# Kernel optimization log

Measured on AMD Instinct MI355X. Metric: run time of the kernel, lower is better.

## Reference

```python
import jax, jax.numpy as jnp
import numpy as np

RADIUS = 0.4
K = 32
EPS = 1e-5


def ball_query(xyz, new_xyz, radius, k):
    """xyz: (B,N,3), new_xyz: (B,M,3) -> idx (B,M,k) int32.
    Replicates CUDA ball_query: first k points within radius (in index order),
    padded with the first found index."""
    N = xyz.shape[1]
    # squared distances (B,M,N)
    d2 = jnp.sum((new_xyz[:, :, None, :] - xyz[:, None, :, :]) ** 2, axis=-1)
    within = d2 < radius * radius
    order = jnp.arange(N, dtype=jnp.int32)
    key = jnp.where(within, order[None, None, :], N)
    idx_sorted = jnp.argsort(key, axis=-1)[..., :k].astype(jnp.int32)  # (B,M,k)
    cnt = within.sum(axis=-1)  # (B,M)
    first = idx_sorted[..., :1]
    slot = jnp.arange(k)[None, None, :]
    return jnp.where(slot < cnt[..., None], idx_sorted, first)


def gather_bmk(x_bnc, idx):
    """x_bnc: (B,N,C), idx: (B,M,K) -> (B,M,K,C)"""
    return jnp.take_along_axis(x_bnc[:, None, :, :], idx[..., None], axis=2)


def conv_bn_relu(x, w, b, gamma, beta):
    """x: (B,Cin,M,K); w: (Cout,Cin). 1x1 Conv2d + BatchNorm2d (train stats) + ReLU."""
    x = jnp.einsum('bcmk,oc->bomk', x, w) + b[None, :, None, None]
    mu = x.mean(axis=(0, 2, 3), keepdims=True)
    var = x.var(axis=(0, 2, 3), keepdims=True)
    x = gamma[None, :, None, None] * (x - mu) * jax.lax.rsqrt(var + EPS) + beta[None, :, None, None]
    return jax.nn.relu(x)


def setup_inputs() -> dict:
    key = jax.random.key(0)
    ks = jax.random.split(key, 16)
    B, N, C, M = 4, 16384, 128, 1024
    mlp = [131, 128, 128, 256]
    inp = {
        'points_xyz': jax.random.normal(ks[0], (B, N, 3), dtype=jnp.float32),
        'features': jax.random.normal(ks[1], (B, C, N), dtype=jnp.float32),
        'indices': jax.random.randint(ks[2], (B, M), 0, N, dtype=jnp.int32),
    }
    for i in range(3):
        cin, cout = mlp[i], mlp[i + 1]
        inp[f'w{i+1}'] = jax.random.normal(ks[3 + 4 * i], (cout, cin), dtype=jnp.float32) / np.sqrt(cin)
        inp[f'b{i+1}'] = jnp.zeros((cout,), dtype=jnp.float32)
        inp[f'g{i+1}'] = jnp.ones((cout,), dtype=jnp.float32)
        inp[f'beta{i+1}'] = jnp.zeros((cout,), dtype=jnp.float32)
    return inp


def reference(points_xyz, features, indices,
              w1, b1, g1, beta1, w2, b2, g2, beta2, w3, b3, g3, beta3):
    # sample centers: new_xyz (B,M,3)
    new_xyz = jnp.take_along_axis(points_xyz, indices[..., None], axis=1)
    # ball query + group
    idx = ball_query(points_xyz, new_xyz, RADIUS, K)            # (B,M,K)
    grouped_xyz = gather_bmk(points_xyz, idx) - new_xyz[:, :, None, :]  # (B,M,K,3)
    grouped_feat = gather_bmk(features.transpose(0, 2, 1), idx)         # (B,M,K,C)
    x = jnp.concatenate([grouped_xyz, grouped_feat], axis=-1)           # (B,M,K,3+C)
    x = x.transpose(0, 3, 1, 2)                                         # (B,3+C,M,K)
    # shared MLP (1x1 Conv2d + BN + ReLU)
    x = conv_bn_relu(x, w1, b1, g1, beta1)
    x = conv_bn_relu(x, w2, b2, g2, beta2)
    x = conv_bn_relu(x, w3, b3, g3, beta3)
    # max pool over K -> (B, Cout, M)
    new_features = x.max(axis=-1)
    return new_xyz, new_features
```

## Files before the change

kernel.cpp:

```cpp
#include <hip/hip_runtime.h>

#define B_ 4
#define N_ 16384
#define C_ 128
#define M_ 1024
#define K_ 32
#define NTOT (B_*M_*K_)
#define RAD2 0.16f
#define EPS_ 1e-5f

typedef unsigned short ushort_t;
typedef __bf16 bf16x8 __attribute__((ext_vector_type(8)));
typedef float f32x4 __attribute__((ext_vector_type(4)));

__device__ __forceinline__ float b2f(ushort_t u){
  unsigned int x = ((unsigned int)u) << 16;
  return __builtin_bit_cast(float, x);
}
__device__ __forceinline__ ushort_t f2b(float f){
  return __builtin_bit_cast(ushort_t, (__bf16)f);
}

__global__ __launch_bounds__(256) void prep_all_k(
    const float* __restrict__ feat, ushort_t* __restrict__ ftr_t,
    const float* __restrict__ xyz, const int* __restrict__ indices,
    float* __restrict__ new_xyz, int* __restrict__ idx,
    const float* __restrict__ w1, const float* __restrict__ w2, const float* __restrict__ w3,
    ushort_t* __restrict__ W1b, ushort_t* __restrict__ W2b, ushort_t* __restrict__ W3b,
    float* __restrict__ stats)
{
  __shared__ float T[32][133];
  int bid = blockIdx.x;
  int t = threadIdx.x;

  if (bid < 2048){
    int b = bid >> 9, ntile = bid & 511;
    int n0 = ntile * 32;
    int nl = t & 31;
    #pragma unroll
    for (int ci = 0; ci < 16; ci++){
      int c = ci*8 + (t >> 5);
      T[nl][c] = feat[((size_t)b*C_ + c)*N_ + n0 + nl];
    }
    __syncthreads();
    #pragma unroll
    for (int ii = 0; ii < 2; ii++){
      int v = ii*256 + t;
      int n2 = v >> 4, seg = v & 15;
      union { ushort_t u[8]; uint4 q; } pk;
      #pragma unroll
      for (int j = 0; j < 8; j++) pk.u[j] = f2b(T[n2][seg*8 + j]);
      *(uint4*)(ftr_t + ((size_t)b*N_ + n0 + n2)*C_ + seg*8) = pk.q;
    }
  } else if (bid < 3072){
    int wv = t >> 6, lane = t & 63;
    int g = (bid - 2048)*4 + wv;
    int b = g >> 10;
    const float* pb = xyz + (size_t)b*N_*3;
    const float4* pb4 = (const float4*)pb;
    int qi = indices[g];
    float qx = pb[qi*3+0], qy = pb[qi*3+1], qz = pb[qi*3+2];
    if (lane < 3) new_xyz[g*3 + lane] = pb[qi*3 + lane];

    int cnt = 0, firstIdx = 0;
    int* op = idx + g*K_;

    float4 buf0[6], buf1[6];
    #pragma unroll
    for (int i = 0; i < 6; i++) buf0[i] = pb4[lane*6 + i];

    auto process = [&](const float4* buf, int chunk){
      const float* f = (const float*)buf;
      unsigned int local_mask = 0;
      #pragma unroll
      for (int j = 0; j < 8; j++){
        float dx = f[j*3+0]-qx, dy = f[j*3+1]-qy, dz = f[j*3+2]-qz;
        if (dx*dx + dy*dy + dz*dz < RAD2) local_mask |= (1u << j);
      }
      if (__ballot(local_mask != 0) == 0ull) return;
      int base = chunk*512;
      int lcnt = __popc(local_mask);
      int incl = lcnt;
      #pragma unroll
      for (int d = 1; d < 64; d <<= 1){
        int tt = __shfl_up(incl, d);
        if (lane >= d) incl += tt;
      }
      int excl = incl - lcnt;
      int total = __shfl(incl, 63);
      if (cnt == 0){
        int lf = local_mask ? (lane*8 + __builtin_ctz(local_mask)) : 0x7fffffff;
        #pragma unroll
        for (int d = 1; d < 64; d <<= 1) lf = min(lf, __shfl_xor(lf, d));
        firstIdx = base + lf;
      }
      int sl = cnt + excl;
      unsigned int m = local_mask;
      while (m && sl < K_){
        int j = __builtin_ctz(m); m &= m - 1u;
        op[sl++] = base + lane*8 + j;
      }
      cnt += total;
    };

    for (int chunk = 0; chunk < 32; chunk += 2){
      if (chunk + 1 < 32){
        #pragma unroll
        for (int i = 0; i < 6; i++) buf1[i] = pb4[(chunk+1)*384 + lane*6 + i];
      }
      process(buf0, chunk);
      if (cnt >= K_) break;
      if (chunk + 2 < 32){
        #pragma unroll
        for (int i = 0; i < 6; i++) buf0[i] = pb4[(chunk+2)*384 + lane*6 + i];
      }
      process(buf1, chunk + 1);
      if (cnt >= K_) break;
    }
    if (cnt < K_){
      for (int s = cnt + lane; s < K_; s += 64) op[s] = firstIdx;
    }
  } else {
    const int T1 = 128*160, T2 = 128*128;
    int e = (bid - 3072)*256 + t;
    if (e < T1){
      int o = e / 160, c = e % 160;
      float v = 0.f;
      if (c < 128) v = w1[o*131 + 3 + c];
      else if (c < 131) v = w1[o*131 + (c - 128)];
      W1b[e] = f2b(v);
    } else if (e < T1+T2){
      int e2 = e - T1;
      W2b[e2] = f2b(w2[e2]);
    } else {
      int e3 = e - T1 - T2;
      W3b[e3] = f2b(w3[e3]);
    }
    if (bid == 3072){
      #pragma unroll
      for (int j = 0; j < 6; j++) stats[j*256 + t] = 0.f;
    }
  }
}

__global__ __launch_bounds__(256, 2) void conv1_k(
    const float* __restrict__ xyz, const ushort_t* __restrict__ ftr_t,
    const int* __restrict__ idx, const float* __restrict__ new_xyz,
    const ushort_t* __restrict__ W1b, const float* __restrict__ b1,
    ushort_t* __restrict__ Y1, float* __restrict__ sumO, float* __restrict__ sqO)
{
  __shared__ alignas(16) ushort_t Xs[2][32*168];
  __shared__ alignas(16) float Ys[2][32*68];
  int t = threadIdx.x;
  int wv = t >> 6, lane = t & 63, quad = lane >> 4, l15 = lane & 15;
  int row = t >> 3, chunk = t & 7;
  int col0 = (blockIdx.x & 1) * 64;
  int blk = blockIdx.x >> 1;

  if (t < 128){
    int rr = t >> 2, cc = t & 3;
    *(uint4*)(Xs[0] + rr*168 + 128 + cc*8) = make_uint4(0,0,0,0);
    *(uint4*)(Xs[1] + rr*168 + 128 + cc*8) = make_uint4(0,0,0,0);
  }
  bf16x8 wf[5];
  #pragma unroll
  for (int kt = 0; kt < 5; kt++)
    wf[kt] = *(const bf16x8*)(W1b + (col0 + wv*16 + l15)*160 + kt*32 + quad*8);
  float bs_r = b1[col0 + wv*16 + l15];
  float s = 0.f, s2 = 0.f;

  const int GPB = 8;
  int g0 = blk * GPB;
  int b = g0 >> 10;
  int ia[GPB], ibv[GPB];
  #pragma unroll
  for (int i = 0; i < GPB; i++){
    ia[i]  = idx[(g0+i)*K_ + row];
    ibv[i] = idx[(g0+i)*K_ + (t & 31)];
  }
  uint4 r0, r1;
  float p3x, p3y, p3z, q3x, q3y, q3z;
  {
    const ushort_t* src = ftr_t + ((size_t)b*N_ + ia[0])*C_ + chunk*16;
    r0 = *(const uint4*)src; r1 = *(const uint4*)(src + 8);
    if (t < 32){
      const float* pp = xyz + ((size_t)b*N_ + ibv[0])*3;
      const float* qq = new_xyz + (size_t)g0*3;
      p3x = pp[0]; p3y = pp[1]; p3z = pp[2];
      q3x = qq[0]; q3y = qq[1]; q3z = qq[2];
    }
  }
  for (int i = 0; i < GPB; i++){
    int p = i & 1;
    ushort_t* X = Xs[p];
    *(uint4*)(X + row*168 + chunk*16) = r0;
    *(uint4*)(X + row*168 + chunk*16 + 8) = r1;
    if (t < 32){
      unsigned int u0 = (unsigned int)f2b(p3x-q3x) | ((unsigned int)f2b(p3y-q3y) << 16);
      unsigned int u1 = (unsigned int)f2b(p3z-q3z);
      *(uint2*)(X + t*168 + 128) = make_uint2(u0, u1);
    }
    if (i + 1 < GPB){
      const ushort_t* src = ftr_t + ((size_t)b*N_ + ia[i+1])*C_ + chunk*16;
      r0 = *(const uint4*)src; r1 = *(const uint4*)(src + 8);
      if (t < 32){
        const float* pp = xyz + ((size_t)b*N_ + ibv[i+1])*3;
        const float* qq = new_xyz + (size_t)(g0+i+1)*3;
        p3x = pp[0]; p3y = pp[1]; p3z = pp[2];
        q3x = qq[0]; q3y = qq[1]; q3z = qq[2];
      }
    }
    __syncthreads();
    bf16x8 af[2][5];
    #pragma unroll
    for (int mt = 0; mt < 2; mt++)
      #pragma unroll
      for (int kt = 0; kt < 5; kt++)
        af[mt][kt] = *(const bf16x8*)(X + (mt*16 + l15)*168 + kt*32 + quad*8);
    f32x4 acc[2] = {(f32x4){0,0,0,0}, (f32x4){0,0,0,0}};
    #pragma unroll
    for (int kt = 0; kt < 5; kt++){
      acc[0] = __builtin_amdgcn_mfma_f32_16x16x32_bf16(af[0][kt], wf[kt], acc[0], 0,0,0);
      acc[1] = __builtin_amdgcn_mfma_f32_16x16x32_bf16(af[1][kt], wf[kt], acc[1], 0,0,0);
    }
    {
      int o = wv*16 + l15;
      float* Yw = Ys[p];
      #pragma unroll
      for (int mt = 0; mt < 2; mt++)
        #pragma unroll
        for (int r = 0; r < 4; r++){
          float v = acc[mt][r] + bs_r;
          s += v; s2 += v*v;
          Yw[(mt*16 + quad*4 + r)*68 + o] = v;
        }
    }
    if (i > 0){
      const float* yp = &Ys[p^1][row*68 + chunk*8];
      f32x4 y0 = *(const f32x4*)(yp);
      f32x4 y1 = *(const f32x4*)(yp + 4);
      union { ushort_t u[8]; uint4 q; } p0;
      #pragma unroll
      for (int j = 0; j < 4; j++){
        p0.u[j] = f2b(y0[j]); p0.u[4+j] = f2b(y1[j]);
      }
      *(uint4*)(Y1 + ((size_t)(g0+i-1)*K_ + row)*128 + col0 + chunk*8) = p0.q;
    }
  }
  __syncthreads();
  {
    const float* yp = &Ys[(GPB-1)&1][row*68 + chunk*8];
    f32x4 y0 = *(const f32x4*)(yp);
    f32x4 y1 = *(const f32x4*)(yp + 4);
    union { ushort_t u[8]; uint4 q; } p0;
    #pragma unroll
    for (int j = 0; j < 4; j++){
      p0.u[j] = f2b(y0[j]); p0.u[4+j] = f2b(y1[j]);
    }
    *(uint4*)(Y1 + ((size_t)(g0+GPB-1)*K_ + row)*128 + col0 + chunk*8) = p0.q;
  }
  s  += __shfl_xor(s, 16);  s  += __shfl_xor(s, 32);
  s2 += __shfl_xor(s2, 16); s2 += __shfl_xor(s2, 32);
  if (quad == 0){
    int o = col0 + wv*16 + l15;
    atomicAdd(&sumO[o], s);
    atomicAdd(&sqO[o], s2);
  }
}

template<int COUT, bool MAXMIN>
__global__ __launch_bounds__(256, 2) void convB_k(
    const ushort_t* __restrict__ Yin, const ushort_t* __restrict__ Wb,
    const float* __restrict__ bias, const float* __restrict__ g_bn,
    const float* __restrict__ beta_bn, const float* __restrict__ sumI,
    const float* __restrict__ sqI, ushort_t* __restrict__ Yout,
    unsigned int* __restrict__ Ymm, float* __restrict__ sumO, float* __restrict__ sqO)
{
  constexpr int HALF = COUT/2;
  constexpr int NT = HALF/64;
  __shared__ alignas(16) ushort_t Xs[2][32*136];
  __shared__ alignas(16) float Ys[MAXMIN ? 1 : 2][MAXMIN ? 4 : 32*68];
  int t = threadIdx.x;
  int wv = t >> 6, lane = t & 63, quad = lane >> 4, l15 = lane & 15;
  int row = t >> 3, chunk = t & 7;
  int col0 = (blockIdx.x & 1) * HALF;
  int blk = blockIdx.x >> 1;

  float a_r[16], d_r[16];
  #pragma unroll
  for (int j = 0; j < 16; j++){
    int c = chunk*16 + j;
    float mu  = sumI[c] * (1.f/NTOT);
    float var = sqI[c]  * (1.f/NTOT) - mu*mu;
    float a = g_bn[c] * rsqrtf(var + EPS_);
    a_r[j] = a; d_r[j] = beta_bn[c] - a*mu;
  }
  bf16x8 wf[NT][4];
  #pragma unroll
  for (int nt = 0; nt < NT; nt++)
    #pragma unroll
    for (int kt = 0; kt < 4; kt++)
      wf[nt][kt] = *(const bf16x8*)(Wb + (col0 + wv*(NT*16) + nt*16 + l15)*128 + kt*32 + quad*8);
  float bs_r[NT];
  #pragma unroll
  for (int nt = 0; nt < NT; nt++) bs_r[nt] = bias[col0 + wv*(NT*16) + nt*16 + l15];
  float s[NT], s2[NT];
  #pragma unroll
  for (int nt = 0; nt < NT; nt++){ s[nt] = 0.f; s2[nt] = 0.f; }

  const int GPB = 8;
  int g0 = blk * GPB;
  uint4 r0, r1;
  {
    const ushort_t* src = Yin + ((size_t)g0*K_ + row)*128 + chunk*16;
    r0 = *(const uint4*)src; r1 = *(const uint4*)(src + 8);
  }
  for (int i = 0; i < GPB; i++){
    int p = i & 1;
    int g = g0 + i;
    ushort_t* X = Xs[p];
    union { ushort_t u[8]; uint4 q; } i0, i1, o0, o1;
    i0.q = r0; i1.q = r1;
    #pragma unroll
    for (int j = 0; j < 8; j++){
      o0.u[j] = f2b(fmaxf(a_r[j]  *b2f(i0.u[j]) + d_r[j],   0.f));
      o1.u[j] = f2b(fmaxf(a_r[8+j]*b2f(i1.u[j]) + d_r[8+j], 0.f));
    }
    *(uint4*)(X + row*136 + chunk*16) = o0.q;
    *(uint4*)(X + row*136 + chunk*16 + 8) = o1.q;
    if (i + 1 < GPB){
      const ushort_t* src = Yin + ((size_t)(g+1)*K_ + row)*128 + chunk*16;
      r0 = *(const uint4*)src; r1 = *(const uint4*)(src + 8);
    }
    __syncthreads();
    bf16x8 af[2][4];
    #pragma unroll
    for (int mt = 0; mt < 2; mt++)
      #pragma unroll
      for (int kt = 0; kt < 4; kt++)
        af[mt][kt] = *(const bf16x8*)(X + (mt*16 + l15)*136 + kt*32 + quad*8);
    f32x4 acc[NT][2];
    #pragma unroll
    for (int nt = 0; nt < NT; nt++){ acc[nt][0] = (f32x4){0,0,0,0}; acc[nt][1] = (f32x4){0,0,0,0}; }
    #pragma unroll
    for (int nt = 0; nt < NT; nt++)
      #pragma unroll
      for (int kt = 0; kt < 4; kt++){
        acc[nt][0] = __builtin_amdgcn_mfma_f32_16x16x32_bf16(af[0][kt], wf[nt][kt], acc[nt][0], 0,0,0);
        acc[nt][1] = __builtin_amdgcn_mfma_f32_16x16x32_bf16(af[1][kt], wf[nt][kt], acc[nt][1], 0,0,0);
      }
    if constexpr (!MAXMIN){
      {
        int o = wv*16 + l15;
        float* Yw = Ys[p];
        #pragma unroll
        for (int mt = 0; mt < 2; mt++)
          #pragma unroll
          for (int r = 0; r < 4; r++){
            float v = acc[0][mt][r] + bs_r[0];
            s[0] += v; s2[0] += v*v;
            Yw[(mt*16 + quad*4 + r)*68 + o] = v;
          }
      }
      if (i > 0){
        const float* yp = &Ys[p^1][row*68 + chunk*8];
        f32x4 y0 = *(const f32x4*)(yp);
        f32x4 y1 = *(const f32x4*)(yp + 4);
        union { ushort_t u[8]; uint4 q; } p0;
        #pragma unroll
        for (int j = 0; j < 4; j++){
          p0.u[j] = f2b(y0[j]); p0.u[4+j] = f2b(y1[j]);
        }
        *(uint4*)(Yout + ((size_t)(g-1)*K_ + row)*128 + col0 + chunk*8) = p0.q;
      }
    } else {
      #pragma unroll
      for (int nt = 0; nt < NT; nt++){
        float v0 = acc[nt][0][0] + bs_r[nt];
        float mx = v0, mn = v0;
        s[nt] += v0; s2[nt] += v0*v0;
        #pragma unroll
        for (int mt = 0; mt < 2; mt++)
          #pragma unroll
          for (int r = 0; r < 4; r++){
            if (mt == 0 && r == 0) continue;
            float v = acc[nt][mt][r] + bs_r[nt];
            s[nt] += v; s2[nt] += v*v;
            mx = fmaxf(mx, v); mn = fminf(mn, v);
          }
        mx = fmaxf(mx, __shfl_xor(mx, 16)); mx = fmaxf(mx, __shfl_xor(mx, 32));
        mn = fminf(mn, __shfl_xor(mn, 16)); mn = fminf(mn, __shfl_xor(mn, 32));
        if (quad == 0){
          int o = col0 + wv*(NT*16) + nt*16 + l15;
          Ymm[(size_t)g*256 + o] = (unsigned int)f2b(mx) | ((unsigned int)f2b(mn) << 16);
        }
      }
    }
  }
  if constexpr (!MAXMIN){
    __syncthreads();
    const float* yp = &Ys[(GPB-1)&1][row*68 + chunk*8];
    f32x4 y0 = *(const f32x4*)(yp);
    f32x4 y1 = *(const f32x4*)(yp + 4);
    union { ushort_t u[8]; uint4 q; } p0;
    #pragma unroll
    for (int j = 0; j < 4; j++){
      p0.u[j] = f2b(y0[j]); p0.u[4+j] = f2b(y1[j]);
    }
    *(uint4*)(Yout + ((size_t)(g0+GPB-1)*K_ + row)*128 + col0 + chunk*8) = p0.q;
  }
  #pragma unroll
  for (int nt = 0; nt < NT; nt++){
    s[nt]  += __shfl_xor(s[nt], 16);  s[nt]  += __shfl_xor(s[nt], 32);
    s2[nt] += __shfl_xor(s2[nt], 16); s2[nt] += __shfl_xor(s2[nt], 32);
    if (quad == 0){
      int o = col0 + wv*(NT*16) + nt*16 + l15;
      atomicAdd(&sumO[o], s[nt]);
      atomicAdd(&sqO[o], s2[nt]);
    }
  }
}

__global__ __launch_bounds__(256) void finalize_k(
    const unsigned int* __restrict__ Ymm, const float* __restrict__ g3,
    const float* __restrict__ beta3, const float* __restrict__ sum3,
    const float* __restrict__ sq3, float* __restrict__ out)
{
  __shared__ float T[16][264];
  __shared__ float abn[256], dbn[256];
  int t = threadIdx.x;
  int b = blockIdx.x >> 6;
  int m0 = (blockIdx.x & 63) * 16;
  {
    float mu  = sum3[t] * (1.f/NTOT);
    float var = sq3[t]  * (1.f/NTOT) - mu*mu;
    float a = g3[t] * rsqrtf(var + EPS_);
    abn[t] = a; dbn[t] = beta3[t] - a*mu;
  }
  __syncthreads();
  #pragma unroll
  for (int i = 0; i < 4; i++){
    int v4 = i*256 + t;
    int m = v4 >> 6, oq = (v4 & 63) * 4;
    uint4 w = *(const uint4*)(Ymm + ((size_t)(b*M_ + m0 + m))*256 + oq);
    unsigned int wsv[4] = {w.x, w.y, w.z, w.w};
    float r[4];
    #pragma unroll
    for (int j = 0; j < 4; j++){
      int o = oq + j;
      float mx = b2f((ushort_t)(wsv[j] & 0xffffu));
      float mn = b2f((ushort_t)(wsv[j] >> 16));
      float a = abn[o];
      float val = (a >= 0.f) ? (a*mx + dbn[o]) : (a*mn + dbn[o]);
      r[j] = fmaxf(val, 0.f);
    }
    *(f32x4*)(&T[m][oq]) = *(f32x4*)r;
  }
  __syncthreads();
  #pragma unroll
  for (int p = 0; p < 4; p++){
    int o = p*64 + (t >> 2), c = t & 3;
    float4 v = make_float4(T[c*4+0][o], T[c*4+1][o], T[c*4+2][o], T[c*4+3][o]);
    *(float4*)(out + ((size_t)(b*256 + o))*M_ + m0 + c*4) = v;
  }
}

extern "C" void kernel_launch(void* const* d_in, const int* in_sizes, int n_in,
                              void* d_out, int out_size, void* d_ws, size_t ws_size,
                              hipStream_t stream)
{
  (void)in_sizes; (void)n_in; (void)out_size; (void)ws_size;
  const float* xyz  = (const float*)d_in[0];
  const float* feat = (const float*)d_in[1];
  const int*   inds = (const int*)d_in[2];
  const float* w1 = (const float*)d_in[3];
  const float* b1 = (const float*)d_in[4];
  const float* g1 = (const float*)d_in[5];
  const float* be1= (const float*)d_in[6];
  const float* w2 = (const float*)d_in[7];
  const float* b2 = (const float*)d_in[8];
  const float* g2 = (const float*)d_in[9];
  const float* be2= (const float*)d_in[10];
  const float* w3 = (const float*)d_in[11];
  const float* b3 = (const float*)d_in[12];
  const float* g3 = (const float*)d_in[13];
  const float* be3= (const float*)d_in[14];

  char* ws = (char*)d_ws;
  float* stats = (float*)ws;
  float* s1sum = stats + 0*256;  float* s1sq = stats + 1*256;
  float* s2sum = stats + 2*256;  float* s2sq = stats + 3*256;
  float* s3sum = stats + 4*256;  float* s3sq = stats + 5*256;
  size_t off = 6*256*sizeof(float);
  int* idx = (int*)(ws + off);                off += (size_t)B_*M_*K_*4;
  ushort_t* ftr_t = (ushort_t*)(ws + off);    off += (size_t)B_*N_*C_*2;
  ushort_t* W1b = (ushort_t*)(ws + off);      off += 128*160*2;
  ushort_t* W2b = (ushort_t*)(ws + off);      off += 128*128*2;
  ushort_t* W3b = (ushort_t*)(ws + off);      off += 256*128*2;
  ushort_t* Y1 = (ushort_t*)(ws + off);       off += (size_t)NTOT*128*2;
  ushort_t* Y2 = (ushort_t*)(ws + off);       off += (size_t)NTOT*128*2;
  unsigned int* Ymm = (unsigned int*)(ws + off); off += (size_t)B_*M_*256*4;

  float* new_xyz  = (float*)d_out;
  float* out_feat = (float*)d_out + (size_t)B_*M_*3;

  prep_all_k<<<3344, 256, 0, stream>>>(feat, ftr_t, xyz, inds, new_xyz, idx,
                                       w1, w2, w3, W1b, W2b, W3b, stats);
  conv1_k<<<1024, 256, 0, stream>>>(xyz, ftr_t, idx, new_xyz, W1b, b1, Y1, s1sum, s1sq);
  convB_k<128,false><<<1024, 256, 0, stream>>>(Y1, W2b, b2, g1, be1, s1sum, s1sq, Y2, nullptr, s2sum, s2sq);
  convB_k<256,true ><<<1024, 256, 0, stream>>>(Y2, W3b, b3, g2, be2, s2sum, s2sq, nullptr, Ymm, s3sum, s3sq);
  finalize_k<<<256, 256, 0, stream>>>(Ymm, g3, be3, s3sum, s3sq, out_feat);
}
```

Measured before the change: 217.6 us.

## Use ballot-based prefix counts in ball query, reorder blocks, raise occupancy bounds

Replaces the shuffle-based prefix scan and min-reduction in the ball query with eight per-bit ballots plus popcounts under a lane mask. It also reorders the prep kernel so the ball-query blocks are dispatched before the feature-transpose blocks, letting the longer-running ball-query waves start first. Separately, it raises the minimum-blocks hint in the launch bounds of conv1 and the convB kernels (to 4 and 4/3) to push the compiler toward fewer registers and higher occupancy. Tighter register budgets risk spills in the MFMA kernels.

```diff
diff --git a/kernel.cpp b/kernel.cpp
--- a/kernel.cpp
+++ b/kernel.cpp
@@ -33,28 +33,9 @@
   int bid = blockIdx.x;
   int t = threadIdx.x;
 
-  if (bid < 2048){
-    int b = bid >> 9, ntile = bid & 511;
-    int n0 = ntile * 32;
-    int nl = t & 31;
-    #pragma unroll
-    for (int ci = 0; ci < 16; ci++){
-      int c = ci*8 + (t >> 5);
-      T[nl][c] = feat[((size_t)b*C_ + c)*N_ + n0 + nl];
-    }
-    __syncthreads();
-    #pragma unroll
-    for (int ii = 0; ii < 2; ii++){
-      int v = ii*256 + t;
-      int n2 = v >> 4, seg = v & 15;
-      union { ushort_t u[8]; uint4 q; } pk;
-      #pragma unroll
-      for (int j = 0; j < 8; j++) pk.u[j] = f2b(T[n2][seg*8 + j]);
-      *(uint4*)(ftr_t + ((size_t)b*N_ + n0 + n2)*C_ + seg*8) = pk.q;
-    }
-  } else if (bid < 3072){
+  if (bid < 1024){
     int wv = t >> 6, lane = t & 63;
-    int g = (bid - 2048)*4 + wv;
+    int g = bid*4 + wv;
     int b = g >> 10;
     const float* pb = xyz + (size_t)b*N_*3;
     const float4* pb4 = (const float4*)pb;
@@ -69,6 +50,8 @@
     #pragma unroll
     for (int i = 0; i < 6; i++) buf0[i] = pb4[lane*6 + i];
 
+    unsigned long long below = (lane == 0) ? 0ull : ((~0ull) >> (64 - lane));
+
     auto process = [&](const float4* buf, int chunk){
       const float* f = (const float*)buf;
       unsigned int local_mask = 0;
@@ -77,22 +60,24 @@
         float dx = f[j*3+0]-qx, dy = f[j*3+1]-qy, dz = f[j*3+2]-qz;
         if (dx*dx + dy*dy + dz*dz < RAD2) local_mask |= (1u << j);
       }
-      if (__ballot(local_mask != 0) == 0ull) return;
+      unsigned long long many = __ballot(local_mask != 0);
+      if (many == 0ull) return;
       int base = chunk*512;
-      int lcnt = __popc(local_mask);
-      int incl = lcnt;
-      #pragma unroll
-      for (int d = 1; d < 64; d <<= 1){
-        int tt = __shfl_up(incl, d);
-        if (lane >= d) incl += tt;
-      }
-      int excl = incl - lcnt;
-      int total = __shfl(incl, 63);
+      unsigned long long mj[8];
+      #pragma unroll
+      for (int j = 0; j < 8; j++) mj[j] = __ballot((local_mask >> j) & 1u);
+      int excl = 0, total = 0;
+      #pragma unroll
+      for (int j = 0; j < 8; j++){
+        excl  += __popcll(mj[j] & below);
+        total += __popcll(mj[j]);
+      }
       if (cnt == 0){
-        int lf = local_mask ? (lane*8 + __builtin_ctz(local_mask)) : 0x7fffffff;
-        #pragma unroll
-        for (int d = 1; d < 64; d <<= 1) lf = min(lf, __shfl_xor(lf, d));
-        firstIdx = base + lf;
+        int l0 = __builtin_ctzll(many);
+        int j0 = 0;
+        #pragma unroll
+        for (int j = 7; j >= 0; j--) if ((mj[j] >> l0) & 1ull) j0 = j;
+        firstIdx = base + l0*8 + j0;
       }
       int sl = cnt + excl;
       unsigned int m = local_mask;
@@ -119,6 +104,26 @@
     }
     if (cnt < K_){
       for (int s = cnt + lane; s < K_; s += 64) op[s] = firstIdx;
+    }
+  } else if (bid < 3072){
+    int bb = bid - 1024;
+    int b = bb >> 9, ntile = bb & 511;
+    int n0 = ntile * 32;
+    int nl = t & 31;
+    #pragma unroll
+    for (int ci = 0; ci < 16; ci++){
+      int c = ci*8 + (t >> 5);
+      T[nl][c] = feat[((size_t)b*C_ + c)*N_ + n0 + nl];
+    }
+    __syncthreads();
+    #pragma unroll
+    for (int ii = 0; ii < 2; ii++){
+      int v = ii*256 + t;
+      int n2 = v >> 4, seg = v & 15;
+      union { ushort_t u[8]; uint4 q; } pk;
+      #pragma unroll
+      for (int j = 0; j < 8; j++) pk.u[j] = f2b(T[n2][seg*8 + j]);
+      *(uint4*)(ftr_t + ((size_t)b*N_ + n0 + n2)*C_ + seg*8) = pk.q;
     }
   } else {
     const int T1 = 128*160, T2 = 128*128;
@@ -143,7 +148,7 @@
   }
 }
 
-__global__ __launch_bounds__(256, 2) void conv1_k(
+__global__ __launch_bounds__(256, 4) void conv1_k(
     const float* __restrict__ xyz, const ushort_t* __restrict__ ftr_t,
     const int* __restrict__ idx, const float* __restrict__ new_xyz,
     const ushort_t* __restrict__ W1b, const float* __restrict__ b1,
@@ -268,8 +273,8 @@
   }
 }
 
-template<int COUT, bool MAXMIN>
-__global__ __launch_bounds__(256, 2) void convB_k(
+template<int COUT, bool MAXMIN, int MINB>
+__global__ __launch_bounds__(256, MINB) void convB_k(
     const ushort_t* __restrict__ Yin, const ushort_t* __restrict__ Wb,
     const float* __restrict__ bias, const float* __restrict__ g_bn,
     const float* __restrict__ beta_bn, const float* __restrict__ sumI,
@@ -507,7 +512,7 @@
   prep_all_k<<<3344, 256, 0, stream>>>(feat, ftr_t, xyz, inds, new_xyz, idx,
                                        w1, w2, w3, W1b, W2b, W3b, stats);
   conv1_k<<<1024, 256, 0, stream>>>(xyz, ftr_t, idx, new_xyz, W1b, b1, Y1, s1sum, s1sq);
-  convB_k<128,false><<<1024, 256, 0, stream>>>(Y1, W2b, b2, g1, be1, s1sum, s1sq, Y2, nullptr, s2sum, s2sq);
-  convB_k<256,true ><<<1024, 256, 0, stream>>>(Y2, W3b, b3, g2, be2, s2sum, s2sq, nullptr, Ymm, s3sum, s3sq);
+  convB_k<128,false,4><<<1024, 256, 0, stream>>>(Y1, W2b, b2, g1, be1, s1sum, s1sq, Y2, nullptr, s2sum, s2sq);
+  convB_k<256,true ,3><<<1024, 256, 0, stream>>>(Y2, W3b, b3, g2, be2, s2sum, s2sq, nullptr, Ymm, s3sum, s3sq);
   finalize_k<<<256, 256, 0, stream>>>(Ymm, g3, be3, s3sum, s3sq, out_feat);
 }
```

New measurement: 211.6 us. 1.03x faster.
